# Optimization experiments

Measured on AMD Instinct MI355X. Metric: run time of the kernel, lower is better.

The kernel has to match this reference:

```python
import jax, jax.numpy as jnp
import numpy as np

# Geometry constants (from init_kwargs)
LO = jnp.array([-51.2, -51.2, -3.0], dtype=jnp.float32)
HI = jnp.array([51.2, 51.2, 3.0], dtype=jnp.float32)
VS = jnp.array([0.2, 0.2, 6.0], dtype=jnp.float32)
NY, NX = 512, 512
BN_EPS = 1e-3  # mmdet3d BN1d default eps


def setup_inputs() -> dict:
    key = jax.random.key(0)
    ks = jax.random.split(key, 11)
    # points uniform inside point_cloud_range -> no points dropped by voxelizer
    points = jax.random.uniform(ks[0], (2, 120000, 3), dtype=jnp.float32) * (HI - LO) + LO
    C2, C = 32, 64
    w0 = jax.random.normal(ks[1], (8, C2), dtype=jnp.float32) / np.sqrt(8.0)
    g0 = jax.random.uniform(ks[2], (C2,), jnp.float32, 0.5, 1.5)
    b0 = jax.random.normal(ks[3], (C2,), jnp.float32) * 0.1
    m0 = jax.random.normal(ks[4], (C2,), jnp.float32) * 0.1
    v0 = jax.random.uniform(ks[5], (C2,), jnp.float32, 0.5, 1.5)
    w1 = jax.random.normal(ks[6], (C, C), dtype=jnp.float32) / np.sqrt(float(C))
    g1 = jax.random.uniform(ks[7], (C,), jnp.float32, 0.5, 1.5)
    b1 = jax.random.normal(ks[8], (C,), jnp.float32) * 0.1
    m1 = jax.random.normal(ks[9], (C,), jnp.float32) * 0.1
    v1 = jax.random.uniform(ks[10], (C,), jnp.float32, 0.5, 1.5)
    return dict(points=points, w0=w0, g0=g0, b0=b0, m0=m0, v0=v0,
                w1=w1, g1=g1, b1=b1, m1=m1, v1=v1)


def _bn(x, g, b, m, v):
    return (x - m) * jax.lax.rsqrt(v + BN_EPS) * g + b


def _embed_one(pts, w0, g0, b0, m0, v0, w1, g1, b1, m1, v1):
    # pts: [N, 3]. Dynamic voxelization: pillar index per point.
    xi = jnp.clip(jnp.floor((pts[:, 0] - LO[0]) / VS[0]).astype(jnp.int32), 0, NX - 1)
    yi = jnp.clip(jnp.floor((pts[:, 1] - LO[1]) / VS[1]).astype(jnp.int32), 0, NY - 1)
    vid = yi * NX + xi                       # flat pillar id, [N]
    nseg = NY * NX
    cnt = jax.ops.segment_sum(jnp.ones_like(pts[:, 0]), vid, nseg)  # [nseg]
    # cluster center offsets (mean xyz per pillar)
    mean = jax.ops.segment_sum(pts, vid, nseg) / jnp.maximum(cnt, 1.0)[:, None]
    f_cluster = pts - mean[vid]              # [N, 3]
    # pillar center offsets (x, y)
    cx = (xi.astype(pts.dtype) + 0.5) * VS[0] + LO[0]
    cy = (yi.astype(pts.dtype) + 0.5) * VS[1] + LO[1]
    f_center = jnp.stack([pts[:, 0] - cx, pts[:, 1] - cy], axis=-1)  # [N, 2]
    feats = jnp.concatenate([pts, f_cluster, f_center], axis=-1)     # [N, 8]
    # PFN layer 0: Linear(no bias) -> BN -> ReLU, then scatter-max + concat back
    h = jax.nn.relu(_bn(feats @ w0, g0, b0, m0, v0))                 # [N, 32]
    pooled0 = jax.ops.segment_max(h, vid, nseg)
    pooled0 = jnp.where(cnt[:, None] > 0, pooled0, 0.0)
    h = jnp.concatenate([h, pooled0[vid]], axis=-1)                  # [N, 64]
    # PFN layer 1 (last): per-point features, then scatter-max -> voxel feats
    h = jax.nn.relu(_bn(h @ w1, g1, b1, m1, v1))                     # [N, 64]
    vox = jax.ops.segment_max(h, vid, nseg)
    vox = jnp.where(cnt[:, None] > 0, vox, 0.0)                      # [nseg, 64]
    # PointPillarsScatter: dense BEV canvas [C, NY, NX]
    canvas = vox.reshape(NY, NX, -1).transpose(2, 0, 1)
    return canvas, h


def reference(points, w0, g0, b0, m0, v0, w1, g1, b1, m1, v1):
    canvases, point_feats = jax.vmap(
        lambda p: _embed_one(p, w0, g0, b0, m0, v0, w1, g1, b1, m1, v1)
    )(points)
    # canvases: [B, C, NY, NX] (torch.cat of per-sample pseudoimages over dim 0)
    return canvases, point_feats
```

## Files before the change

### kernel.cpp

```cpp
#include <hip/hip_runtime.h>

#define NPT   120000
#define NB    2
#define NSEG  262144
#define NXg   512
#define NSEGT (NB * NSEG)

typedef __attribute__((ext_vector_type(8))) short  bf16x8;
typedef __attribute__((ext_vector_type(4))) float  f32x4;

__device__ __forceinline__ unsigned short f2bf(float f) {
    unsigned u = __float_as_uint(f);
    return (unsigned short)((u + 0x7FFFu + ((u >> 16) & 1u)) >> 16);
}

__global__ __launch_bounds__(256) void k_stats(const float* __restrict__ pts,
                                               unsigned int* __restrict__ cnt,
                                               int* __restrict__ vids,
                                               unsigned int* __restrict__ rank) {
    int tid = blockIdx.x * 256 + threadIdx.x;
    if (tid >= NB * NPT) return;
    const float* p = pts + (size_t)tid * 3;
    float x = p[0], y = p[1];
    int xi = (int)floorf((x - (-51.2f)) / 0.2f);
    int yi = (int)floorf((y - (-51.2f)) / 0.2f);
    xi = min(max(xi, 0), 511);
    yi = min(max(yi, 0), 511);
    int b = (tid >= NPT) ? 1 : 0;
    int gvid = b * NSEG + (yi * NXg + xi);
    vids[tid] = gvid;
    rank[tid] = atomicAdd(&cnt[gvid], 1u);
}

__global__ __launch_bounds__(256) void k_scan1(const unsigned int* __restrict__ cnt,
                                               unsigned int* __restrict__ offs,
                                               unsigned int* __restrict__ bsum) {
    __shared__ unsigned int s[256];
    int t = threadIdx.x;
    size_t base = (size_t)blockIdx.x * 1024 + t * 4;
    uint4 c4 = *(const uint4*)(cnt + base);
    unsigned int tsum = c4.x + c4.y + c4.z + c4.w;
    s[t] = tsum;
    __syncthreads();
    for (int o = 1; o < 256; o <<= 1) {
        unsigned int v = (t >= o) ? s[t - o] : 0u;
        __syncthreads();
        s[t] += v;
        __syncthreads();
    }
    unsigned int pre = s[t] - tsum;
    if (t == 255) bsum[blockIdx.x] = s[255];
    uint4 o4;
    o4.x = pre; o4.y = pre + c4.x; o4.z = o4.y + c4.y; o4.w = o4.z + c4.z;
    *(uint4*)(offs + base) = o4;
}

__global__ __launch_bounds__(256) void k_scan2(unsigned int* __restrict__ bsum) {
    __shared__ unsigned int s[256];
    int t = threadIdx.x;
    unsigned int a = bsum[2 * t], b = bsum[2 * t + 1];
    unsigned int ts = a + b;
    s[t] = ts;
    __syncthreads();
    for (int o = 1; o < 256; o <<= 1) {
        unsigned int v = (t >= o) ? s[t - o] : 0u;
        __syncthreads();
        s[t] += v;
        __syncthreads();
    }
    unsigned int pre = s[t] - ts;
    bsum[2 * t] = pre;
    bsum[2 * t + 1] = pre + a;
}

__global__ __launch_bounds__(256) void k_scan3(unsigned int* __restrict__ offs,
                                               const unsigned int* __restrict__ bsum) {
    size_t base = (size_t)blockIdx.x * 1024 + threadIdx.x * 4;
    unsigned int add = bsum[blockIdx.x];
    uint4 o4 = *(uint4*)(offs + base);
    o4.x += add; o4.y += add; o4.z += add; o4.w += add;
    *(uint4*)(offs + base) = o4;
}

__global__ __launch_bounds__(256) void k_reorder(const float* __restrict__ pts,
                                                 const int* __restrict__ vids,
                                                 const unsigned int* __restrict__ rank,
                                                 const unsigned int* __restrict__ offs,
                                                 float4* __restrict__ sxyz,
                                                 int* __restrict__ posvid,
                                                 int* __restrict__ ptofpos) {
    int tid = blockIdx.x * 256 + threadIdx.x;
    if (tid >= NB * NPT) return;
    const float* p = pts + (size_t)tid * 3;
    int gvid = vids[tid];
    unsigned pos = offs[gvid] + rank[tid];
    sxyz[pos] = make_float4(p[0], p[1], p[2], __int_as_float(gvid));
    posvid[pos] = gvid;
    ptofpos[pos] = tid;
}

__global__ __launch_bounds__(256) void k_prep(const float* __restrict__ w1,
                                              const float* __restrict__ g1,
                                              const float* __restrict__ b1,
                                              const float* __restrict__ m1,
                                              const float* __restrict__ v1,
                                              unsigned short* __restrict__ wtbf,
                                              float* __restrict__ bias1f) {
    int t = threadIdx.x;
    #pragma unroll
    for (int i = 0; i < 16; ++i) {
        int idx = t + i * 256;
        int c = idx >> 6, k = idx & 63;
        float al = g1[c] * rsqrtf(v1[c] + 1e-3f);
        wtbf[idx] = f2bf(w1[k * 64 + c] * al);
    }
    if (t < 64) bias1f[t] = b1[t] - m1[t] * (g1[t] * rsqrtf(v1[t] + 1e-3f));
}

__global__ __launch_bounds__(256) void k_pfn0(const float4* __restrict__ sxyz,
                                              const unsigned int* __restrict__ offs,
                                              const unsigned int* __restrict__ cnt,
                                              const float* __restrict__ w0,
                                              const float* __restrict__ g0,
                                              const float* __restrict__ b0,
                                              const float* __restrict__ m0,
                                              const float* __restrict__ v0,
                                              unsigned short* __restrict__ xbf) {
    __shared__ float w0f[256];
    __shared__ float bias0[32];
    int t = threadIdx.x;
    {
        int c = t & 31;
        float al = g0[c] * rsqrtf(v0[c] + 1e-3f);
        w0f[t] = w0[t] * al;
        if (t < 32) bias0[t] = b0[t] - m0[t] * al;
    }
    __syncthreads();

    int pos = blockIdx.x * 256 + t;
    if (pos >= NB * NPT) return;

    float4 me = sxyz[pos];
    float x = me.x, y = me.y, z = me.z;
    int gvid = __float_as_int(me.w);
    int vid = gvid & (NSEG - 1);
    int xi = vid & (NXg - 1), yi = vid >> 9;

    unsigned off = offs[gvid];
    unsigned n   = cnt[gvid];
    float sx = 0.f, sy = 0.f, sz = 0.f;
    for (unsigned i = 0; i < n; ++i) {
        float4 q = sxyz[off + i];
        sx += q.x; sy += q.y; sz += q.z;
    }
    float inv = 1.0f / (float)n;
    float mx = sx * inv, my = sy * inv, mz = sz * inv;
    float cx = ((float)xi + 0.5f) * 0.2f + (-51.2f);
    float cy = ((float)yi + 0.5f) * 0.2f + (-51.2f);

    float f[8] = {x, y, z, x - mx, y - my, z - mz, x - cx, y - cy};

    unsigned wv[16];
    #pragma unroll
    for (int c2 = 0; c2 < 16; ++c2) {
        float a0 = bias0[2 * c2], a1 = bias0[2 * c2 + 1];
        #pragma unroll
        for (int k = 0; k < 8; ++k) {
            a0 += f[k] * w0f[k * 32 + 2 * c2];
            a1 += f[k] * w0f[k * 32 + 2 * c2 + 1];
        }
        unsigned lo = f2bf(fmaxf(a0, 0.0f));
        unsigned hi = f2bf(fmaxf(a1, 0.0f));
        wv[c2] = lo | (hi << 16);
    }
    uint4* dst = (uint4*)(xbf + (size_t)pos * 64);
    dst[0] = make_uint4(wv[0], wv[1], wv[2], wv[3]);
    dst[1] = make_uint4(wv[4], wv[5], wv[6], wv[7]);
    dst[2] = make_uint4(wv[8], wv[9], wv[10], wv[11]);
    dst[3] = make_uint4(wv[12], wv[13], wv[14], wv[15]);
}

__global__ __launch_bounds__(256) void k_pfn1(const unsigned short* __restrict__ xbf,
                                              const int* __restrict__ posvid,
                                              const int* __restrict__ ptofpos,
                                              const unsigned int* __restrict__ offs,
                                              const unsigned int* __restrict__ cnt,
                                              const unsigned short* __restrict__ wtbf,
                                              const float* __restrict__ bias1f,
                                              float* __restrict__ ptfeat,
                                              float* __restrict__ canvas) {
    __shared__ unsigned pooled[64][32];
    __shared__ unsigned short xlds[64 * 64];
    __shared__ unsigned voxl[64][65];
    __shared__ int origarr[64];
    __shared__ unsigned char vlocarr[64];

    int t = threadIdx.x;
    int l = t & 63;
    int w = t >> 6;

    int batch = blockIdx.x >> 12;
    int vid0 = (blockIdx.x & 4095) << 6;
    int gvid0 = batch * NSEG + vid0;

    for (int i = t; i < 64 * 32; i += 256) ((unsigned*)pooled)[i] = 0u;
    for (int i = t; i < 64 * 65; i += 256) ((unsigned*)voxl)[i] = 0u;

    unsigned poslo = offs[gvid0];
    unsigned poshi = offs[gvid0 + 63] + cnt[gvid0 + 63];

    bf16x8 bfr[4][2];
    float bia[4];
    #pragma unroll
    for (int n = 0; n < 4; ++n) {
        #pragma unroll
        for (int ks = 0; ks < 2; ++ks)
            bfr[n][ks] = *(const bf16x8*)(wtbf + ((n * 16 + (l & 15)) * 64 +
                                                  ks * 32 + (l >> 4) * 8));
        bia[n] = bias1f[n * 16 + (l & 15)];
    }
    __syncthreads();

    {
        int k = t & 31, g = t >> 5;
        for (unsigned p = poslo + g; p < poshi; p += 8) {
            int vloc = (posvid[p] & (NSEG - 1)) - vid0;
            unsigned u = xbf[(size_t)p * 64 + k];
            atomicMax(&pooled[vloc][k], u << 16);
        }
    }
    __syncthreads();

    for (unsigned pc = poslo; pc < poshi; pc += 64) {
        unsigned m = min(64u, poshi - pc);

        for (int idx = t; idx < 512; idx += 256) {
            int pt = idx >> 3, seg = idx & 7;
            unsigned lin = (unsigned)(pt * 128 + seg * 16);
            unsigned swz = lin ^ ((unsigned)(pt & 7) << 4);
            bf16x8 val;
            #pragma unroll
            for (int e = 0; e < 8; ++e) val[e] = 0;
            if (pt < (int)m) {
                unsigned p = pc + pt;
                if (seg < 4) {
                    val = *(const bf16x8*)(xbf + (size_t)p * 64 + seg * 8);
                } else {
                    int vloc = (posvid[p] & (NSEG - 1)) - vid0;
                    #pragma unroll
                    for (int e = 0; e < 8; ++e)
                        val[e] = (short)(pooled[vloc][(seg - 4) * 8 + e] >> 16);
                    if (seg == 4) {
                        vlocarr[pt] = (unsigned char)vloc;
                        origarr[pt] = ptofpos[p];
                    }
                }
            }
            *(bf16x8*)((char*)xlds + swz) = val;
        }
        __syncthreads();

        {
            int row = w * 16 + (l & 15);
            unsigned base = (unsigned)(row * 128 + ((l >> 4) << 4));
            unsigned sw = (unsigned)(row & 7) << 4;
            bf16x8 a0 = *(const bf16x8*)((char*)xlds + ((base + 0) ^ sw));
            bf16x8 a1 = *(const bf16x8*)((char*)xlds + ((base + 64) ^ sw));
            #pragma unroll
            for (int n = 0; n < 4; ++n) {
                f32x4 acc = {0.f, 0.f, 0.f, 0.f};
                acc = __builtin_amdgcn_mfma_f32_16x16x32_bf16(a0, bfr[n][0], acc, 0, 0, 0);
                acc = __builtin_amdgcn_mfma_f32_16x16x32_bf16(a1, bfr[n][1], acc, 0, 0, 0);
                int ch = n * 16 + (l & 15);
                #pragma unroll
                for (int r = 0; r < 4; ++r) {
                    int pidx = w * 16 + (l >> 4) * 4 + r;
                    float v = fmaxf(acc[r] + bia[n], 0.0f);
                    if (pidx < (int)m) {
                        ptfeat[(size_t)origarr[pidx] * 64 + ch] = v;
                        atomicMax(&voxl[vlocarr[pidx]][ch], __float_as_uint(v));
                    }
                }
            }
        }
        __syncthreads();
    }

    {
        float* cv = canvas + (size_t)batch * 64 * NSEG + vid0;
        int p = l;
        #pragma unroll
        for (int i = 0; i < 16; ++i) {
            int c = i * 4 + w;
            cv[(size_t)c * NSEG + p] = __uint_as_float(voxl[p][c]);
        }
    }
}

extern "C" void kernel_launch(void* const* d_in, const int* in_sizes, int n_in,
                              void* d_out, int out_size, void* d_ws, size_t ws_size,
                              hipStream_t stream) {
    const float* pts = (const float*)d_in[0];
    const float* w0  = (const float*)d_in[1];
    const float* g0  = (const float*)d_in[2];
    const float* b0  = (const float*)d_in[3];
    const float* m0  = (const float*)d_in[4];
    const float* v0  = (const float*)d_in[5];
    const float* w1  = (const float*)d_in[6];
    const float* g1  = (const float*)d_in[7];
    const float* b1  = (const float*)d_in[8];
    const float* m1  = (const float*)d_in[9];
    const float* v1  = (const float*)d_in[10];
    float* out = (float*)d_out;
    float* ptfeat = out + (size_t)NB * 64 * NSEG;

    char* ws = (char*)d_ws;
    size_t off = 0;
    unsigned int* cnt   = (unsigned int*)(ws + off); off += (size_t)NSEGT * 4;
    unsigned int* offs  = (unsigned int*)(ws + off); off += (size_t)NSEGT * 4;
    int* vids           = (int*)(ws + off);          off += (size_t)NB * NPT * 4;
    unsigned int* rank  = (unsigned int*)(ws + off); off += (size_t)NB * NPT * 4;
    int* posvid         = (int*)(ws + off);          off += (size_t)NB * NPT * 4;
    int* ptofpos        = (int*)(ws + off);          off += (size_t)NB * NPT * 4;
    float4* sxyz        = (float4*)(ws + off);       off += (size_t)NB * NPT * 16;
    unsigned short* xbf = (unsigned short*)(ws + off); off += (size_t)NB * NPT * 64 * 2;
    unsigned short* wtbf= (unsigned short*)(ws + off); off += 4096 * 2;
    float* bias1f       = (float*)(ws + off);        off += 64 * 4;
    unsigned int* bsum  = (unsigned int*)(ws + off); off += 512 * 4;

    hipMemsetAsync(cnt, 0, (size_t)NSEGT * 4, stream);

    int npts = NB * NPT;
    int nblk = (npts + 255) / 256;
    k_stats<<<nblk, 256, 0, stream>>>(pts, cnt, vids, rank);
    k_scan1<<<NSEGT / 1024, 256, 0, stream>>>(cnt, offs, bsum);
    k_scan2<<<1, 256, 0, stream>>>(bsum);
    k_scan3<<<NSEGT / 1024, 256, 0, stream>>>(offs, bsum);
    k_reorder<<<nblk, 256, 0, stream>>>(pts, vids, rank, offs, sxyz, posvid, ptofpos);
    k_prep<<<1, 256, 0, stream>>>(w1, g1, b1, m1, v1, wtbf, bias1f);
    k_pfn0<<<nblk, 256, 0, stream>>>(sxyz, offs, cnt, w0, g0, b0, m0, v0, xbf);
    k_pfn1<<<NB * 4096, 256, 0, stream>>>(xbf, posvid, ptofpos, offs, cnt,
                                          wtbf, bias1f, ptfeat, out);
}
```

Measured before the change: 129.4 us.

## Fuse pooling into pfn0, merge init kernels, drop scan3 and index arrays

Replaces the memset and the prep kernel with one init kernel, and removes the scan3 pass by adding the block sums at read time. The reorder kernel recomputes voxel ids instead of reading them back, and packs the local voxel slot and the original point index into one combined word. pfn0 now computes layer-0 features for every point in its pillar and writes both its own features and the pooled max into a 64-wide bf16 row, so pfn1 no longer needs a shared-memory pooling pass with atomics. The cost is redundant per-pillar recomputation in pfn0, which grows quadratically with pillar occupancy, though occupancy is low here.

```diff
diff --git a/kernel.cpp b/kernel.cpp
--- a/kernel.cpp
+++ b/kernel.cpp
@@ -5,6 +5,7 @@
 #define NSEG  262144
 #define NXg   512
 #define NSEGT (NB * NSEG)
+#define NPTS  (NB * NPT)
 
 typedef __attribute__((ext_vector_type(8))) short  bf16x8;
 typedef __attribute__((ext_vector_type(4))) float  f32x4;
@@ -14,12 +15,35 @@
     return (unsigned short)((u + 0x7FFFu + ((u >> 16) & 1u)) >> 16);
 }
 
+__global__ __launch_bounds__(256) void k_init(unsigned int* __restrict__ cnt,
+                                              const float* __restrict__ w1,
+                                              const float* __restrict__ g1,
+                                              const float* __restrict__ b1,
+                                              const float* __restrict__ m1,
+                                              const float* __restrict__ v1,
+                                              unsigned short* __restrict__ wtbf,
+                                              float* __restrict__ bias1f) {
+    int t = threadIdx.x;
+    if (blockIdx.x < 512) {
+        int idx = blockIdx.x * 256 + t;
+        ((uint4*)cnt)[idx] = make_uint4(0u, 0u, 0u, 0u);
+        return;
+    }
+    #pragma unroll
+    for (int i = 0; i < 16; ++i) {
+        int idx = t + i * 256;
+        int c = idx >> 6, k = idx & 63;
+        float al = g1[c] * rsqrtf(v1[c] + 1e-3f);
+        wtbf[idx] = f2bf(w1[k * 64 + c] * al);
+    }
+    if (t < 64) bias1f[t] = b1[t] - m1[t] * (g1[t] * rsqrtf(v1[t] + 1e-3f));
+}
+
 __global__ __launch_bounds__(256) void k_stats(const float* __restrict__ pts,
                                                unsigned int* __restrict__ cnt,
-                                               int* __restrict__ vids,
                                                unsigned int* __restrict__ rank) {
     int tid = blockIdx.x * 256 + threadIdx.x;
-    if (tid >= NB * NPT) return;
+    if (tid >= NPTS) return;
     const float* p = pts + (size_t)tid * 3;
     float x = p[0], y = p[1];
     int xi = (int)floorf((x - (-51.2f)) / 0.2f);
@@ -28,7 +52,6 @@
     yi = min(max(yi, 0), 511);
     int b = (tid >= NPT) ? 1 : 0;
     int gvid = b * NSEG + (yi * NXg + xi);
-    vids[tid] = gvid;
     rank[tid] = atomicAdd(&cnt[gvid], 1u);
 }
 
@@ -73,52 +96,30 @@
     bsum[2 * t + 1] = pre + a;
 }
 
-__global__ __launch_bounds__(256) void k_scan3(unsigned int* __restrict__ offs,
-                                               const unsigned int* __restrict__ bsum) {
-    size_t base = (size_t)blockIdx.x * 1024 + threadIdx.x * 4;
-    unsigned int add = bsum[blockIdx.x];
-    uint4 o4 = *(uint4*)(offs + base);
-    o4.x += add; o4.y += add; o4.z += add; o4.w += add;
-    *(uint4*)(offs + base) = o4;
-}
-
 __global__ __launch_bounds__(256) void k_reorder(const float* __restrict__ pts,
-                                                 const int* __restrict__ vids,
                                                  const unsigned int* __restrict__ rank,
                                                  const unsigned int* __restrict__ offs,
+                                                 const unsigned int* __restrict__ bsum,
                                                  float4* __restrict__ sxyz,
-                                                 int* __restrict__ posvid,
-                                                 int* __restrict__ ptofpos) {
+                                                 unsigned int* __restrict__ comb) {
     int tid = blockIdx.x * 256 + threadIdx.x;
-    if (tid >= NB * NPT) return;
+    if (tid >= NPTS) return;
     const float* p = pts + (size_t)tid * 3;
-    int gvid = vids[tid];
-    unsigned pos = offs[gvid] + rank[tid];
-    sxyz[pos] = make_float4(p[0], p[1], p[2], __int_as_float(gvid));
-    posvid[pos] = gvid;
-    ptofpos[pos] = tid;
-}
-
-__global__ __launch_bounds__(256) void k_prep(const float* __restrict__ w1,
-                                              const float* __restrict__ g1,
-                                              const float* __restrict__ b1,
-                                              const float* __restrict__ m1,
-                                              const float* __restrict__ v1,
-                                              unsigned short* __restrict__ wtbf,
-                                              float* __restrict__ bias1f) {
-    int t = threadIdx.x;
-    #pragma unroll
-    for (int i = 0; i < 16; ++i) {
-        int idx = t + i * 256;
-        int c = idx >> 6, k = idx & 63;
-        float al = g1[c] * rsqrtf(v1[c] + 1e-3f);
-        wtbf[idx] = f2bf(w1[k * 64 + c] * al);
-    }
-    if (t < 64) bias1f[t] = b1[t] - m1[t] * (g1[t] * rsqrtf(v1[t] + 1e-3f));
+    float x = p[0], y = p[1], z = p[2];
+    int xi = (int)floorf((x - (-51.2f)) / 0.2f);
+    int yi = (int)floorf((y - (-51.2f)) / 0.2f);
+    xi = min(max(xi, 0), 511);
+    yi = min(max(yi, 0), 511);
+    int b = (tid >= NPT) ? 1 : 0;
+    int gvid = b * NSEG + (yi * NXg + xi);
+    unsigned pos = offs[gvid] + bsum[gvid >> 10] + rank[tid];
+    sxyz[pos] = make_float4(x, y, z, __int_as_float(gvid));
+    comb[pos] = ((unsigned)(gvid & 63) << 18) | (unsigned)tid;
 }
 
 __global__ __launch_bounds__(256) void k_pfn0(const float4* __restrict__ sxyz,
                                               const unsigned int* __restrict__ offs,
+                                              const unsigned int* __restrict__ bsum,
                                               const unsigned int* __restrict__ cnt,
                                               const float* __restrict__ w0,
                                               const float* __restrict__ g0,
@@ -138,15 +139,14 @@
     __syncthreads();
 
     int pos = blockIdx.x * 256 + t;
-    if (pos >= NB * NPT) return;
+    if (pos >= NPTS) return;
 
     float4 me = sxyz[pos];
-    float x = me.x, y = me.y, z = me.z;
     int gvid = __float_as_int(me.w);
     int vid = gvid & (NSEG - 1);
     int xi = vid & (NXg - 1), yi = vid >> 9;
 
-    unsigned off = offs[gvid];
+    unsigned off = offs[gvid] + bsum[gvid >> 10];
     unsigned n   = cnt[gvid];
     float sx = 0.f, sy = 0.f, sz = 0.f;
     for (unsigned i = 0; i < n; ++i) {
@@ -158,42 +158,54 @@
     float cx = ((float)xi + 0.5f) * 0.2f + (-51.2f);
     float cy = ((float)yi + 0.5f) * 0.2f + (-51.2f);
 
-    float f[8] = {x, y, z, x - mx, y - my, z - mz, x - cx, y - cy};
+    float own[32], pool[32];
+    #pragma unroll
+    for (int c = 0; c < 32; ++c) { pool[c] = 0.0f; own[c] = 0.0f; }
+    for (unsigned i = 0; i < n; ++i) {
+        float4 q = sxyz[off + i];
+        float f[8] = {q.x, q.y, q.z, q.x - mx, q.y - my, q.z - mz,
+                      q.x - cx, q.y - cy};
+        bool self = (off + i == (unsigned)pos);
+        #pragma unroll
+        for (int c = 0; c < 32; ++c) {
+            float acc = bias0[c];
+            #pragma unroll
+            for (int k = 0; k < 8; ++k) acc += f[k] * w0f[k * 32 + c];
+            acc = fmaxf(acc, 0.0f);
+            pool[c] = fmaxf(pool[c], acc);
+            if (self) own[c] = acc;
+        }
+    }
 
     unsigned wv[16];
-    #pragma unroll
-    for (int c2 = 0; c2 < 16; ++c2) {
-        float a0 = bias0[2 * c2], a1 = bias0[2 * c2 + 1];
-        #pragma unroll
-        for (int k = 0; k < 8; ++k) {
-            a0 += f[k] * w0f[k * 32 + 2 * c2];
-            a1 += f[k] * w0f[k * 32 + 2 * c2 + 1];
-        }
-        unsigned lo = f2bf(fmaxf(a0, 0.0f));
-        unsigned hi = f2bf(fmaxf(a1, 0.0f));
-        wv[c2] = lo | (hi << 16);
-    }
     uint4* dst = (uint4*)(xbf + (size_t)pos * 64);
-    dst[0] = make_uint4(wv[0], wv[1], wv[2], wv[3]);
-    dst[1] = make_uint4(wv[4], wv[5], wv[6], wv[7]);
-    dst[2] = make_uint4(wv[8], wv[9], wv[10], wv[11]);
+    #pragma unroll
+    for (int c2 = 0; c2 < 16; ++c2)
+        wv[c2] = (unsigned)f2bf(own[2 * c2]) | ((unsigned)f2bf(own[2 * c2 + 1]) << 16);
+    dst[0] = make_uint4(wv[0],  wv[1],  wv[2],  wv[3]);
+    dst[1] = make_uint4(wv[4],  wv[5],  wv[6],  wv[7]);
+    dst[2] = make_uint4(wv[8],  wv[9],  wv[10], wv[11]);
     dst[3] = make_uint4(wv[12], wv[13], wv[14], wv[15]);
+    #pragma unroll
+    for (int c2 = 0; c2 < 16; ++c2)
+        wv[c2] = (unsigned)f2bf(pool[2 * c2]) | ((unsigned)f2bf(pool[2 * c2 + 1]) << 16);
+    dst[4] = make_uint4(wv[0],  wv[1],  wv[2],  wv[3]);
+    dst[5] = make_uint4(wv[4],  wv[5],  wv[6],  wv[7]);
+    dst[6] = make_uint4(wv[8],  wv[9],  wv[10], wv[11]);
+    dst[7] = make_uint4(wv[12], wv[13], wv[14], wv[15]);
 }
 
 __global__ __launch_bounds__(256) void k_pfn1(const unsigned short* __restrict__ xbf,
-                                              const int* __restrict__ posvid,
-                                              const int* __restrict__ ptofpos,
+                                              const unsigned int* __restrict__ comb,
                                               const unsigned int* __restrict__ offs,
-                                              const unsigned int* __restrict__ cnt,
+                                              const unsigned int* __restrict__ bsum,
                                               const unsigned short* __restrict__ wtbf,
                                               const float* __restrict__ bias1f,
                                               float* __restrict__ ptfeat,
                                               float* __restrict__ canvas) {
-    __shared__ unsigned pooled[64][32];
     __shared__ unsigned short xlds[64 * 64];
     __shared__ unsigned voxl[64][65];
-    __shared__ int origarr[64];
-    __shared__ unsigned char vlocarr[64];
+    __shared__ unsigned combs[64];
 
     int t = threadIdx.x;
     int l = t & 63;
@@ -203,11 +215,15 @@
     int vid0 = (blockIdx.x & 4095) << 6;
     int gvid0 = batch * NSEG + vid0;
 
-    for (int i = t; i < 64 * 32; i += 256) ((unsigned*)pooled)[i] = 0u;
-    for (int i = t; i < 64 * 65; i += 256) ((unsigned*)voxl)[i] = 0u;
-
-    unsigned poslo = offs[gvid0];
-    unsigned poshi = offs[gvid0 + 63] + cnt[gvid0 + 63];
+    #pragma unroll
+    for (int i = 0; i < 17; ++i) {
+        int idx = t + i * 256;
+        if (idx < 64 * 65) ((unsigned*)voxl)[idx] = 0u;
+    }
+
+    unsigned poslo = offs[gvid0] + bsum[gvid0 >> 10];
+    int g2 = gvid0 + 64;
+    unsigned poshi = (g2 < NSEGT) ? offs[g2] + bsum[g2 >> 10] : (unsigned)NPTS;
 
     bf16x8 bfr[4][2];
     float bia[4];
@@ -218,16 +234,6 @@
             bfr[n][ks] = *(const bf16x8*)(wtbf + ((n * 16 + (l & 15)) * 64 +
                                                   ks * 32 + (l >> 4) * 8));
         bia[n] = bias1f[n * 16 + (l & 15)];
-    }
-    __syncthreads();
-
-    {
-        int k = t & 31, g = t >> 5;
-        for (unsigned p = poslo + g; p < poshi; p += 8) {
-            int vloc = (posvid[p] & (NSEG - 1)) - vid0;
-            unsigned u = xbf[(size_t)p * 64 + k];
-            atomicMax(&pooled[vloc][k], u << 16);
-        }
     }
     __syncthreads();
 
@@ -241,23 +247,11 @@
             bf16x8 val;
             #pragma unroll
             for (int e = 0; e < 8; ++e) val[e] = 0;
-            if (pt < (int)m) {
-                unsigned p = pc + pt;
-                if (seg < 4) {
-                    val = *(const bf16x8*)(xbf + (size_t)p * 64 + seg * 8);
-                } else {
-                    int vloc = (posvid[p] & (NSEG - 1)) - vid0;
-                    #pragma unroll
-                    for (int e = 0; e < 8; ++e)
-                        val[e] = (short)(pooled[vloc][(seg - 4) * 8 + e] >> 16);
-                    if (seg == 4) {
-                        vlocarr[pt] = (unsigned char)vloc;
-                        origarr[pt] = ptofpos[p];
-                    }
-                }
-            }
+            if (pt < (int)m)
+                val = *(const bf16x8*)(xbf + (size_t)(pc + pt) * 64 + seg * 8);
             *(bf16x8*)((char*)xlds + swz) = val;
         }
+        for (int pt = t; pt < (int)m; pt += 256) combs[pt] = comb[pc + pt];
         __syncthreads();
 
         {
@@ -275,10 +269,11 @@
                 #pragma unroll
                 for (int r = 0; r < 4; ++r) {
                     int pidx = w * 16 + (l >> 4) * 4 + r;
-                    float v = fmaxf(acc[r] + bia[n], 0.0f);
                     if (pidx < (int)m) {
-                        ptfeat[(size_t)origarr[pidx] * 64 + ch] = v;
-                        atomicMax(&voxl[vlocarr[pidx]][ch], __float_as_uint(v));
+                        unsigned u = combs[pidx];
+                        float v = fmaxf(acc[r] + bia[n], 0.0f);
+                        ptfeat[(size_t)(u & 0x3FFFFu) * 64 + ch] = v;
+                        atomicMax(&voxl[u >> 18][ch], __float_as_uint(v));
                     }
                 }
             }
@@ -288,11 +283,10 @@
 
     {
         float* cv = canvas + (size_t)batch * 64 * NSEG + vid0;
-        int p = l;
         #pragma unroll
         for (int i = 0; i < 16; ++i) {
             int c = i * 4 + w;
-            cv[(size_t)c * NSEG + p] = __uint_as_float(voxl[p][c]);
+            cv[(size_t)c * NSEG + l] = __uint_as_float(voxl[l][c]);
         }
     }
 }
@@ -318,27 +312,22 @@
     size_t off = 0;
     unsigned int* cnt   = (unsigned int*)(ws + off); off += (size_t)NSEGT * 4;
     unsigned int* offs  = (unsigned int*)(ws + off); off += (size_t)NSEGT * 4;
-    int* vids           = (int*)(ws + off);          off += (size_t)NB * NPT * 4;
-    unsigned int* rank  = (unsigned int*)(ws + off); off += (size_t)NB * NPT * 4;
-    int* posvid         = (int*)(ws + off);          off += (size_t)NB * NPT * 4;
-    int* ptofpos        = (int*)(ws + off);          off += (size_t)NB * NPT * 4;
-    float4* sxyz        = (float4*)(ws + off);       off += (size_t)NB * NPT * 16;
-    unsigned short* xbf = (unsigned short*)(ws + off); off += (size_t)NB * NPT * 64 * 2;
+    unsigned int* rank  = (unsigned int*)(ws + off); off += (size_t)NPTS * 4;
+    unsigned int* comb  = (unsigned int*)(ws + off); off += (size_t)NPTS * 4;
+    float4* sxyz        = (float4*)(ws + off);       off += (size_t)NPTS * 16;
+    unsigned short* xbf = (unsigned short*)(ws + off); off += (size_t)NPTS * 64 * 2;
     unsigned short* wtbf= (unsigned short*)(ws + off); off += 4096 * 2;
     float* bias1f       = (float*)(ws + off);        off += 64 * 4;
     unsigned int* bsum  = (unsigned int*)(ws + off); off += 512 * 4;
 
-    hipMemsetAsync(cnt, 0, (size_t)NSEGT * 4, stream);
-
-    int npts = NB * NPT;
-    int nblk = (npts + 255) / 256;
-    k_stats<<<nblk, 256, 0, stream>>>(pts, cnt, vids, rank);
+    int nblk = (NPTS + 255) / 256;
+    k_init<<<513, 256, 0, stream>>>(cnt, w1, g1, b1, m1, v1, wtbf, bias1f);
+    k_stats<<<nblk, 256, 0, stream>>>(pts, cnt, rank);
     k_scan1<<<NSEGT / 1024, 256, 0, stream>>>(cnt, offs, bsum);
     k_scan2<<<1, 256, 0, stream>>>(bsum);
-    k_scan3<<<NSEGT / 1024, 256, 0, stream>>>(offs, bsum);
-    k_reorder<<<nblk, 256, 0, stream>>>(pts, vids, rank, offs, sxyz, posvid, ptofpos);
-    k_prep<<<1, 256, 0, stream>>>(w1, g1, b1, m1, v1, wtbf, bias1f);
-    k_pfn0<<<nblk, 256, 0, stream>>>(sxyz, offs, cnt, w0, g0, b0, m0, v0, xbf);
-    k_pfn1<<<NB * 4096, 256, 0, stream>>>(xbf, posvid, ptofpos, offs, cnt,
+    k_reorder<<<nblk, 256, 0, stream>>>(pts, rank, offs, bsum, sxyz, comb);
+    k_pfn0<<<nblk, 256, 0, stream>>>(sxyz, offs, bsum, cnt,
+                                     w0, g0, b0, m0, v0, xbf);
+    k_pfn1<<<NB * 4096, 256, 0, stream>>>(xbf, comb, offs, bsum,
                                           wtbf, bias1f, ptfeat, out);
 }
```

Measured after the change: 129.0 us. Within noise of the previous version (-0.3%).
